# Kernel tuning notes

Measured on AMD Instinct MI355X. Metric: run time of the kernel, lower is better.

## Reference

```python
import jax, jax.numpy as jnp
import numpy as np

B, T, D = 8, 2048, 1024
GAMMA = 0.96875


def setup_inputs() -> dict:
    key = jax.random.key(0)
    ks = jax.random.split(key, 7)
    sD = 1.0 / np.sqrt(D)
    sT = 1.0 / np.sqrt(T)
    return {
        "x": jax.random.normal(ks[0], (B, T, D), dtype=jnp.float32),
        "Wq": jax.random.normal(ks[1], (D, D), dtype=jnp.float32) * sD,
        "Wk": jax.random.normal(ks[2], (D, D), dtype=jnp.float32) * sD,
        "Wv": jax.random.normal(ks[3], (D, D), dtype=jnp.float32) * sD,
        "W_ih": jax.random.normal(ks[4], (T, T), dtype=jnp.float32) * sT,
        "W_hh": jax.random.normal(ks[5], (T, T), dtype=jnp.float32) * sT,
        "b_ih": jax.random.normal(ks[6], (T,), dtype=jnp.float32) * sT,
    }


def reference(x, Wq, Wk, Wv, W_ih, W_hh, b_ih):
    # x: [B, T, D]; QKV projections (Linear with no bias: x @ W^T)
    Q = jnp.einsum("btd,ed->bte", x, Wq)
    K = jnp.einsum("btd,ed->bte", x, Wk)
    V = jnp.einsum("btd,ed->bte", x, Wv)

    # retention state injected as hidden bias of the tanh-RNN: [B, T]
    bias = jnp.sum(K * V, axis=-1)

    gamma = jnp.full((T,), GAMMA, dtype=x.dtype)
    u = gamma @ W_ih.T + b_ih  # input contribution, identical every step: [T]

    def step(h, b_t):
        h_new = jnp.tanh(u + h @ W_hh.T + b_t)
        return h_new, h_new

    h0 = jnp.zeros((T,), dtype=x.dtype)
    _, S = jax.lax.scan(step, h0, bias)  # scan over the B rows -> S: [B, T]

    # vmap(mul)(S, Q^T)^T  ==  out[b,t,d] = S[b,t] * Q[b,t,d]
    return S[:, :, None] * Q
```

## Files before the change

### kernel.cpp

```cpp
#include <hip/hip_runtime.h>
#include <stdint.h>

#define T_DIM 2048
#define D_DIM 1024
#define B_DIM 8
#define M_TOK (B_DIM * T_DIM)
#define GAMMA_C 0.96875f

typedef float f32x4 __attribute__((ext_vector_type(4)));
typedef float f32x16 __attribute__((ext_vector_type(16)));
typedef float fl4 __attribute__((ext_vector_type(4)));
typedef __bf16 bf16x8 __attribute__((ext_vector_type(8)));
typedef unsigned short us8 __attribute__((ext_vector_type(8)));
typedef unsigned short us4 __attribute__((ext_vector_type(4)));

__device__ __forceinline__ unsigned short f32_bf16_rne(float f) {
  uint32_t u = __builtin_bit_cast(uint32_t, f);
  return (unsigned short)((u + 0x7FFFu + ((u >> 16) & 1u)) >> 16);
}
__device__ __forceinline__ float bf16_f32(unsigned short h) {
  uint32_t u = ((uint32_t)h) << 16;
  return __builtin_bit_cast(float, u);
}

__device__ __forceinline__ int swz_row(int r) {
  return ((r >> 1) & 3) ^ ((r >> 3) & 3);
}

__device__ __forceinline__ void gload16(const void* g, void* l) {
  __builtin_amdgcn_global_load_lds(
      reinterpret_cast<const __attribute__((address_space(1))) uint32_t*>(
          reinterpret_cast<uintptr_t>(g)),
      reinterpret_cast<__attribute__((address_space(3))) uint32_t*>(
          reinterpret_cast<uintptr_t>(l)),
      16, 0, 0);
}

__device__ __forceinline__ bf16x8 ldfrag(const unsigned short* p) {
  us8 u = *reinterpret_cast<const us8*>(p);
  return __builtin_bit_cast(bf16x8, u);
}

#define VMW(n) asm volatile("s_waitcnt vmcnt(" #n ")" ::: "memory")
#define BAR    __builtin_amdgcn_s_barrier()

__global__ __launch_bounds__(256) void k_split(const float* __restrict__ in, int n8,
                                               unsigned short* __restrict__ hi,
                                               unsigned short* __restrict__ lo) {
  int stride = gridDim.x * blockDim.x;
  for (int i = blockIdx.x * blockDim.x + threadIdx.x; i < n8; i += stride) {
    fl4 v0 = ((const fl4*)in)[i * 2];
    fl4 v1 = ((const fl4*)in)[i * 2 + 1];
    us8 h, l;
#pragma unroll
    for (int j = 0; j < 4; ++j) {
      unsigned short hb = f32_bf16_rne(v0[j]);
      h[j] = hb;
      l[j] = f32_bf16_rne(v0[j] - bf16_f32(hb));
      unsigned short hb1 = f32_bf16_rne(v1[j]);
      h[j + 4] = hb1;
      l[j + 4] = f32_bf16_rne(v1[j] - bf16_f32(hb1));
    }
    ((us8*)hi)[i] = h;
    ((us8*)lo)[i] = l;
  }
}

__global__ __launch_bounds__(256) void k_split_hi(const float* __restrict__ in, int n8,
                                                  unsigned short* __restrict__ hi) {
  int stride = gridDim.x * blockDim.x;
  for (int i = blockIdx.x * blockDim.x + threadIdx.x; i < n8; i += stride) {
    fl4 v0 = ((const fl4*)in)[i * 2];
    fl4 v1 = ((const fl4*)in)[i * 2 + 1];
    us8 h;
#pragma unroll
    for (int j = 0; j < 4; ++j) {
      h[j] = f32_bf16_rne(v0[j]);
      h[j + 4] = f32_bf16_rne(v1[j]);
    }
    ((us8*)hi)[i] = h;
  }
}

__global__ __launch_bounds__(256) void k_split_T(const float* __restrict__ in,
                                                 unsigned short* __restrict__ th,
                                                 unsigned short* __restrict__ tl) {
  __shared__ float tile[64][69];
  int be = blockIdx.x >> 4, bd = blockIdx.x & 15;
  int e0 = be * 64, d0 = bd * 64;
  int r = threadIdx.x >> 4;
  int c = (threadIdx.x & 15) * 4;
#pragma unroll
  for (int it = 0; it < 4; ++it) {
    int rr = r + it * 16;
    fl4 v = *(const fl4*)(in + (size_t)(e0 + rr) * D_DIM + d0 + c);
#pragma unroll
    for (int j = 0; j < 4; ++j) tile[rr][c + j] = v[j];
  }
  __syncthreads();
#pragma unroll
  for (int it = 0; it < 4; ++it) {
    int dr = r + it * 16;
    us4 h, l;
#pragma unroll
    for (int j = 0; j < 4; ++j) {
      float f = tile[c + j][dr];
      h[j] = f32_bf16_rne(f);
      l[j] = f32_bf16_rne(f - bf16_f32(h[j]));
    }
    *(us4*)(th + (size_t)(d0 + dr) * D_DIM + e0 + c) = h;
    *(us4*)(tl + (size_t)(d0 + dr) * D_DIM + e0 + c) = l;
  }
}

__global__ __launch_bounds__(256) void k_u(const float* __restrict__ Wih,
                                           const float* __restrict__ bih,
                                           float* __restrict__ u) {
  int wave = threadIdx.x >> 6, lane = threadIdx.x & 63;
  int t = blockIdx.x * 4 + wave;
  const fl4* row = (const fl4*)(Wih + (size_t)t * T_DIM);
  float s = 0.f;
#pragma unroll
  for (int i = 0; i < 8; ++i) {
    fl4 v = row[lane + i * 64];
    s += v[0] + v[1] + v[2] + v[3];
  }
#pragma unroll
  for (int m = 32; m >= 1; m >>= 1) s += __shfl_xor(s, m, 64);
  if (lane == 0) u[t] = GAMMA_C * s + bih[t];
}

__global__ __launch_bounds__(256) void k_step_bf(const unsigned short* __restrict__ Whh_b,
                                                 const float* __restrict__ hprev,
                                                 const float* __restrict__ u,
                                                 const float* __restrict__ biasrow,
                                                 float* __restrict__ hout) {
  int wave = threadIdx.x >> 6, lane = threadIdx.x & 63;
  int t = blockIdx.x * 4 + wave;
  const unsigned short* row = Whh_b + (size_t)t * T_DIM;
  float s = 0.f;
#pragma unroll
  for (int i = 0; i < 4; ++i) {
    us8 w = *(const us8*)(row + i * 512 + lane * 8);
    fl4 h0 = *(const fl4*)(hprev + i * 512 + lane * 8);
    fl4 h1 = *(const fl4*)(hprev + i * 512 + lane * 8 + 4);
    s += bf16_f32(w[0]) * h0[0] + bf16_f32(w[1]) * h0[1] +
         bf16_f32(w[2]) * h0[2] + bf16_f32(w[3]) * h0[3] +
         bf16_f32(w[4]) * h1[0] + bf16_f32(w[5]) * h1[1] +
         bf16_f32(w[6]) * h1[2] + bf16_f32(w[7]) * h1[3];
  }
#pragma unroll
  for (int m = 32; m >= 1; m >>= 1) s += __shfl_xor(s, m, 64);
  if (lane == 0) hout[t] = tanhf(u[t] + s + biasrow[t]);
}

__global__ __launch_bounds__(256) void k_ht(
    const unsigned short* __restrict__ ah, const unsigned short* __restrict__ al,
    const unsigned short* __restrict__ bh, const unsigned short* __restrict__ bl,
    float* __restrict__ Hf) {
  __shared__ unsigned short sAh[2][64 * 32], sAl[2][64 * 32];
  __shared__ unsigned short sBh[2][64 * 32], sBl[2][64 * 32];
  const int tid = threadIdx.x;
  const int wave = tid >> 6, lane = tid & 63;
  const int wm = wave >> 1, wn = wave & 1;
  const int m0 = (blockIdx.x >> 4) * 64, n0 = (blockIdx.x & 15) * 64;
  const int hi32 = lane >> 5;

  const int srow = tid >> 2;
  const int csrc = (tid & 3) ^ swz_row(srow);
  const size_t ga = (size_t)(m0 + srow) * D_DIM + csrc * 8;
  const size_t gb = (size_t)(n0 + srow) * D_DIM + csrc * 8;
  const int ldst = tid * 8;

  f32x16 acc = {};
  const int l31 = lane & 31;
  const int sw = swz_row(l31);
  const int ar = wm * 32 + l31;
  const int br = wn * 32 + l31;
  int aoff[2], boff[2];
#pragma unroll
  for (int kh = 0; kh < 2; ++kh) {
    aoff[kh] = ar * 32 + (((kh * 2 + hi32) ^ sw) * 8);
    boff[kh] = br * 32 + (((kh * 2 + hi32) ^ sw) * 8);
  }

  auto stage = [&](int t, int buf) {
    const size_t ko = (size_t)t * 32;
    gload16(ah + ga + ko, &sAh[buf][ldst]);
    gload16(al + ga + ko, &sAl[buf][ldst]);
    gload16(bh + gb + ko, &sBh[buf][ldst]);
    gload16(bl + gb + ko, &sBl[buf][ldst]);
  };

  stage(0, 0);
  stage(1, 1);
  for (int kt = 0; kt < 32; ++kt) {
    const int cur = kt & 1;
    if (kt < 31) { VMW(4); } else { VMW(0); }
    BAR;
#pragma unroll
    for (int kh = 0; kh < 2; ++kh) {
      bf16x8 fah = ldfrag(&sAh[cur][aoff[kh]]);
      bf16x8 fal = ldfrag(&sAl[cur][aoff[kh]]);
      bf16x8 fbh = ldfrag(&sBh[cur][boff[kh]]);
      bf16x8 fbl = ldfrag(&sBl[cur][boff[kh]]);
      acc = __builtin_amdgcn_mfma_f32_32x32x16_bf16(fah, fbh, acc, 0, 0, 0);
      acc = __builtin_amdgcn_mfma_f32_32x32x16_bf16(fah, fbl, acc, 0, 0, 0);
      acc = __builtin_amdgcn_mfma_f32_32x32x16_bf16(fal, fbh, acc, 0, 0, 0);
    }
    BAR;
    if (kt + 2 <= 31) stage(kt + 2, cur);
  }
#pragma unroll
  for (int r = 0; r < 16; ++r) {
    int row = m0 + wm * 32 + (r & 3) + 8 * (r >> 2) + 4 * hi32;
    int col = n0 + wn * 32 + l31;
    Hf[(size_t)row * D_DIM + col] = acc[r];
  }
}

__global__ __launch_bounds__(256) void k_nprime(const float* __restrict__ Hf,
                                                unsigned short* __restrict__ mh,
                                                unsigned short* __restrict__ ml) {
  __shared__ float t2[64][65];
  const int ti = blockIdx.x >> 4;
  const int tj = blockIdx.x & 15;
  const int r0 = ti * 64, c0 = tj * 64;
  const int a = threadIdx.x >> 2;
  const int b4 = (threadIdx.x & 3) * 16;
  if (tj < ti) {
#pragma unroll
    for (int j = 0; j < 16; ++j) {
      size_t ad = (size_t)(r0 + a) * D_DIM + c0 + b4 + j;
      mh[ad] = 0;
      ml[ad] = 0;
    }
    return;
  }
#pragma unroll
  for (int j = 0; j < 16; j += 4) {
    fl4 v = *(const fl4*)(Hf + (size_t)(c0 + a) * D_DIM + r0 + b4 + j);
#pragma unroll
    for (int q = 0; q < 4; ++q) t2[a][b4 + j + q] = v[q];
  }
  __syncthreads();
#pragma unroll
  for (int j = 0; j < 16; ++j) {
    int dp = r0 + a;
    int dd = c0 + b4 + j;
    float v = 0.f;
    if (dd > dp)       v = Hf[(size_t)dp * D_DIM + dd] + t2[b4 + j][a];
    else if (dd == dp) v = Hf[(size_t)dp * D_DIM + dd];
    unsigned short hb = f32_bf16_rne(v);
    unsigned short lb = f32_bf16_rne(v - bf16_f32(hb));
    size_t ad = (size_t)dp * D_DIM + dd;
    mh[ad] = hb;
    ml[ad] = lb;
  }
}

__global__ __launch_bounds__(512, 1) void k_y_bias(
    const unsigned short* __restrict__ xh, const unsigned short* __restrict__ xl,
    const unsigned short* __restrict__ bh, const unsigned short* __restrict__ bl,
    float* __restrict__ bias) {
  __shared__ unsigned short sAh[3][128 * 32], sAl[3][128 * 32];
  __shared__ unsigned short sBh[3][256 * 32], sBl[3][256 * 32];
  const int tid = threadIdx.x;
  const int wave = tid >> 6, lane = tid & 63;
  const int wm = wave >> 2;
  const int wn = wave & 3;
  const int xcd = blockIdx.x & 7, seq = blockIdx.x >> 3;
  const int mb = xcd * 16 + (seq >> 1);
  const int half = seq & 1;
  const int m0 = mb * 128;
  const int l15 = lane & 15;
  const int kc = lane >> 4;

  const int srow = tid >> 2;
  const int csrc = (tid & 3) ^ swz_row(srow);
  const size_t gA = (size_t)(m0 + srow) * D_DIM + csrc * 8;
  const int ldstA = tid * 8;
  const int ldstB0 = tid * 8, ldstB1 = (tid + 512) * 8;

  int aoff[4], boff[4];
#pragma unroll
  for (int mi = 0; mi < 4; ++mi) {
    int r = wm * 64 + mi * 16 + l15;
    aoff[mi] = r * 32 + ((kc ^ swz_row(r)) * 8);
  }
#pragma unroll
  for (int ni = 0; ni < 4; ++ni) {
    int r = wn * 64 + ni * 16 + l15;
    boff[ni] = r * 32 + ((kc ^ swz_row(r)) * 8);
  }

  auto phase = [&](int nb, int k0, int ke) {
    const int n0 = nb * 256;
    const size_t gB0 = (size_t)(n0 + srow) * D_DIM + csrc * 8;
    const size_t gB1 = (size_t)(n0 + srow + 128) * D_DIM + csrc * 8;

    auto stage = [&](int t, int buf) {
      const size_t ko = (size_t)t * 32;
      gload16(xh + gA + ko, &sAh[buf][ldstA]);
      gload16(xl + gA + ko, &sAl[buf][ldstA]);
      gload16(bh + gB0 + ko, &sBh[buf][ldstB0]);
      gload16(bh + gB1 + ko, &sBh[buf][ldstB1]);
      gload16(bl + gB0 + ko, &sBl[buf][ldstB0]);
      gload16(bl + gB1 + ko, &sBl[buf][ldstB1]);
    };

    f32x4 acc[4][4] = {};
    BAR;
    stage(k0, 0);
    stage(k0 + 1, 1);
    int cur = 0;
    for (int kt = k0; kt < ke; ++kt) {
      if (kt < ke - 1) { VMW(6); } else { VMW(0); }
      BAR;
      int nx = cur + 2; if (nx >= 3) nx -= 3;
      if (kt + 2 < ke) stage(kt + 2, nx);
      {
        bf16x8 fah[4], fal[4];
#pragma unroll
        for (int mi = 0; mi < 4; ++mi) {
          fah[mi] = ldfrag(&sAh[cur][aoff[mi]]);
          fal[mi] = ldfrag(&sAl[cur][aoff[mi]]);
        }
#pragma unroll
        for (int nh = 0; nh < 2; ++nh) {
          bf16x8 fbh_[2], fbl_[2];
#pragma unroll
          for (int nj = 0; nj < 2; ++nj) {
            fbh_[nj] = ldfrag(&sBh[cur][boff[nh * 2 + nj]]);
            fbl_[nj] = ldfrag(&sBl[cur][boff[nh * 2 + nj]]);
          }
          __builtin_amdgcn_s_setprio(1);
#pragma unroll
          for (int mi = 0; mi < 4; ++mi)
#pragma unroll
            for (int nj = 0; nj < 2; ++nj) {
              const int ni = nh * 2 + nj;
              acc[mi][ni] = __builtin_amdgcn_mfma_f32_16x16x32_bf16(fah[mi], fbh_[nj], acc[mi][ni], 0, 0, 0);
              acc[mi][ni] = __builtin_amdgcn_mfma_f32_16x16x32_bf16(fah[mi], fbl_[nj], acc[mi][ni], 0, 0, 0);
              acc[mi][ni] = __builtin_amdgcn_mfma_f32_16x16x32_bf16(fal[mi], fbh_[nj], acc[mi][ni], 0, 0, 0);
            }
          __builtin_amdgcn_s_setprio(0);
        }
      }
      cur = cur + 1; if (cur >= 3) cur -= 3;
    }

#pragma unroll
    for (int mi = 0; mi < 4; ++mi)
#pragma unroll
      for (int j = 0; j < 4; ++j) {
        int row = m0 + wm * 64 + mi * 16 + (lane >> 4) * 4 + j;
        const size_t rb = (size_t)row * D_DIM + n0 + wn * 64 + l15;
        float p = 0.f;
#pragma unroll
        for (int ni = 0; ni < 4; ++ni) {
          float xv = bf16_f32(xh[rb + ni * 16]) + bf16_f32(xl[rb + ni * 16]);
          p += xv * acc[mi][ni][j];
        }
        p += __shfl_xor(p, 1, 64);
        p += __shfl_xor(p, 2, 64);
        p += __shfl_xor(p, 4, 64);
        p += __shfl_xor(p, 8, 64);
        if (l15 == 0) atomicAdd(&bias[row], p);
      }
  };

  if (half == 0) {
    phase(0, 0, 32);
    phase(1, 8, 16);
  } else {
    phase(1, 16, 32);
    phase(2, 16, 32);
    phase(3, 24, 32);
  }
}

__global__ __launch_bounds__(256, 4) void k_q_out(
    const unsigned short* __restrict__ xh,
    const unsigned short* __restrict__ qh_,
    const float* __restrict__ S, float* __restrict__ out) {
  __shared__ unsigned short sA[2][128 * 32];
  __shared__ unsigned short sB[2][128 * 32];
  const int tid = threadIdx.x;
  const int wave = tid >> 6, lane = tid & 63;
  const int wm = wave >> 1, wn = wave & 1;
  int sw0 = (blockIdx.x & 7) * 128 + (blockIdx.x >> 3);
  const int mb = sw0 >> 3, nb = sw0 & 7;
  const int m0 = mb * 128, n0 = nb * 128;
  const int hi32 = lane >> 5;
  const int l31 = lane & 31;

  const int srow0 = tid >> 2, srow1 = srow0 + 64;
  const int csrc0 = (tid & 3) ^ swz_row(srow0);
  const int csrc1 = (tid & 3) ^ swz_row(srow1);
  const size_t gaA0 = (size_t)(m0 + srow0) * D_DIM + csrc0 * 8;
  const size_t gaA1 = (size_t)(m0 + srow1) * D_DIM + csrc1 * 8;
  const size_t gaB0 = (size_t)(n0 + srow0) * D_DIM + csrc0 * 8;
  const size_t gaB1 = (size_t)(n0 + srow1) * D_DIM + csrc1 * 8;
  const int ldst0 = tid * 8, ldst1 = (tid + 256) * 8;

  f32x16 acc[2][2] = {};
  int aoff[2][2], boff[2][2];
#pragma unroll
  for (int mi = 0; mi < 2; ++mi) {
    int r = wm * 64 + mi * 32 + l31;
    int sw = swz_row(r);
#pragma unroll
    for (int kh = 0; kh < 2; ++kh)
      aoff[mi][kh] = r * 32 + (((kh * 2 + hi32) ^ sw) * 8);
  }
#pragma unroll
  for (int ni = 0; ni < 2; ++ni) {
    int r = wn * 64 + ni * 32 + l31;
    int sw = swz_row(r);
#pragma unroll
    for (int kh = 0; kh < 2; ++kh)
      boff[ni][kh] = r * 32 + (((kh * 2 + hi32) ^ sw) * 8);
  }

  auto stage = [&](int t, int buf) {
    const size_t ko = (size_t)t * 32;
    gload16(xh + gaA0 + ko, &sA[buf][ldst0]);
    gload16(xh + gaA1 + ko, &sA[buf][ldst1]);
    gload16(qh_ + gaB0 + ko, &sB[buf][ldst0]);
    gload16(qh_ + gaB1 + ko, &sB[buf][ldst1]);
  };

  stage(0, 0);
  stage(1, 1);
  for (int kt = 0; kt < 32; ++kt) {
    const int cur = kt & 1;
    if (kt < 31) { VMW(4); } else { VMW(0); }
    BAR;
#pragma unroll
    for (int kh = 0; kh < 2; ++kh) {
      bf16x8 fa[2], fb[2];
#pragma unroll
      for (int mi = 0; mi < 2; ++mi) fa[mi] = ldfrag(&sA[cur][aoff[mi][kh]]);
#pragma unroll
      for (int ni = 0; ni < 2; ++ni) fb[ni] = ldfrag(&sB[cur][boff[ni][kh]]);
      __builtin_amdgcn_s_setprio(1);
#pragma unroll
      for (int mi = 0; mi < 2; ++mi)
#pragma unroll
        for (int ni = 0; ni < 2; ++ni)
          acc[mi][ni] = __builtin_amdgcn_mfma_f32_32x32x16_bf16(fa[mi], fb[ni], acc[mi][ni], 0, 0, 0);
      __builtin_amdgcn_s_setprio(0);
    }
    BAR;
    if (kt + 2 <= 31) stage(kt + 2, cur);
  }

#pragma unroll
  for (int mi = 0; mi < 2; ++mi)
#pragma unroll
    for (int r = 0; r < 16; ++r) {
      int row = m0 + wm * 64 + mi * 32 + (r & 3) + 8 * (r >> 2) + 4 * hi32;
      float sc = S[row];
      float* orow = out + (size_t)row * D_DIM + n0 + wn * 64 + l31;
      orow[0] = sc * acc[mi][0][r];
      orow[32] = sc * acc[mi][1][r];
    }
}

extern "C" void kernel_launch(void* const* d_in, const int* in_sizes, int n_in,
                              void* d_out, int out_size, void* d_ws, size_t ws_size,
                              hipStream_t stream) {
  const float* x   = (const float*)d_in[0];
  const float* Wq  = (const float*)d_in[1];
  const float* Wk  = (const float*)d_in[2];
  const float* Wv  = (const float*)d_in[3];
  const float* Wih = (const float*)d_in[4];
  const float* Whh = (const float*)d_in[5];
  const float* bih = (const float*)d_in[6];
  float* out = (float*)d_out;

  char* ws = (char*)d_ws;
  size_t off = 0;
  auto alloc = [&](size_t bytes) -> char* {
    char* p = ws + off;
    off += (bytes + 255) & ~(size_t)255;
    return p;
  };
  unsigned short* xh   = (unsigned short*)alloc((size_t)M_TOK * D_DIM * 2);
  unsigned short* xl   = (unsigned short*)alloc((size_t)M_TOK * D_DIM * 2);
  unsigned short* wqh  = (unsigned short*)alloc((size_t)D_DIM * D_DIM * 2);
  unsigned short* wkth = (unsigned short*)alloc((size_t)D_DIM * D_DIM * 2);
  unsigned short* wktl = (unsigned short*)alloc((size_t)D_DIM * D_DIM * 2);
  unsigned short* wvth = (unsigned short*)alloc((size_t)D_DIM * D_DIM * 2);
  unsigned short* wvtl = (unsigned short*)alloc((size_t)D_DIM * D_DIM * 2);
  unsigned short* mph  = (unsigned short*)alloc((size_t)D_DIM * D_DIM * 2);
  unsigned short* mpl  = (unsigned short*)alloc((size_t)D_DIM * D_DIM * 2);
  float* Hf   = (float*)alloc((size_t)D_DIM * D_DIM * 4);
  float* bias = (float*)alloc((size_t)M_TOK * 4);
  float* Sbuf = (float*)alloc((size_t)M_TOK * 4);
  float* ubuf = (float*)alloc((size_t)T_DIM * 4);
  float* zbuf = (float*)alloc((size_t)T_DIM * 4);
  unsigned short* whhb = wkth;
  (void)ws_size; (void)in_sizes; (void)n_in; (void)out_size;

  k_split<<<2048, 256, 0, stream>>>(x, M_TOK * D_DIM / 8, xh, xl);
  k_split_hi<<<512, 256, 0, stream>>>(Wq, D_DIM * D_DIM / 8, wqh);
  k_split_T<<<256, 256, 0, stream>>>(Wk, wkth, wktl);
  k_split_T<<<256, 256, 0, stream>>>(Wv, wvth, wvtl);

  hipMemsetAsync(bias, 0, (size_t)M_TOK * 4, stream);
  hipMemsetAsync(zbuf, 0, (size_t)T_DIM * 4, stream);

  k_u<<<T_DIM / 4, 256, 0, stream>>>(Wih, bih, ubuf);

  k_ht<<<256, 256, 0, stream>>>(wvth, wvtl, wkth, wktl, Hf);

  k_nprime<<<256, 256, 0, stream>>>(Hf, mph, mpl);

  k_split_hi<<<1024, 256, 0, stream>>>(Whh, T_DIM * T_DIM / 8, whhb);

  k_y_bias<<<256, 512, 0, stream>>>(xh, xl, mph, mpl, bias);

  for (int b = 0; b < B_DIM; ++b) {
    const float* hp = (b == 0) ? zbuf : (Sbuf + (size_t)(b - 1) * T_DIM);
    k_step_bf<<<T_DIM / 4, 256, 0, stream>>>(whhb, hp, ubuf, bias + (size_t)b * T_DIM,
                                             Sbuf + (size_t)b * T_DIM);
  }

  k_q_out<<<1024, 256, 0, stream>>>(xh, wqh, Sbuf, out);
}
```

Before: 238.6 us.

## Enlarge k_y_bias tile to 256x256 with 1024 threads and double buffering

Restructures the bias GEMM kernel to use 1024-thread blocks, each covering a 256-row M tile instead of 128. The LDS pipeline goes from triple to double buffering, with an extra barrier before the next prefetch. The upper-triangular work is rebalanced across four quarters per M block instead of two halves. The aim is better reuse of the B tile and more even work per block, at the cost of less prefetch depth, an added barrier per k-step, and tighter per-thread register budget.

```diff
diff --git a/kernel.cpp b/kernel.cpp
--- a/kernel.cpp
+++ b/kernel.cpp
@@ -43,6 +43,7 @@
 
 #define VMW(n) asm volatile("s_waitcnt vmcnt(" #n ")" ::: "memory")
 #define BAR    __builtin_amdgcn_s_barrier()
+#define MEMFENCE asm volatile("" ::: "memory")
 
 __global__ __launch_bounds__(256) void k_split(const float* __restrict__ in, int n8,
                                                unsigned short* __restrict__ hi,
@@ -259,28 +260,27 @@
   }
 }
 
-__global__ __launch_bounds__(512, 1) void k_y_bias(
+__global__ __launch_bounds__(1024, 1) void k_y_bias(
     const unsigned short* __restrict__ xh, const unsigned short* __restrict__ xl,
     const unsigned short* __restrict__ bh, const unsigned short* __restrict__ bl,
     float* __restrict__ bias) {
-  __shared__ unsigned short sAh[3][128 * 32], sAl[3][128 * 32];
-  __shared__ unsigned short sBh[3][256 * 32], sBl[3][256 * 32];
+  __shared__ unsigned short sAh[2][256 * 32], sAl[2][256 * 32];
+  __shared__ unsigned short sBh[2][256 * 32], sBl[2][256 * 32];
   const int tid = threadIdx.x;
   const int wave = tid >> 6, lane = tid & 63;
   const int wm = wave >> 2;
   const int wn = wave & 3;
   const int xcd = blockIdx.x & 7, seq = blockIdx.x >> 3;
-  const int mb = xcd * 16 + (seq >> 1);
-  const int half = seq & 1;
-  const int m0 = mb * 128;
+  const int mb = xcd * 8 + (seq >> 2);
+  const int quarter = seq & 3;
+  const int m0 = mb * 256;
   const int l15 = lane & 15;
   const int kc = lane >> 4;
 
   const int srow = tid >> 2;
   const int csrc = (tid & 3) ^ swz_row(srow);
   const size_t gA = (size_t)(m0 + srow) * D_DIM + csrc * 8;
-  const int ldstA = tid * 8;
-  const int ldstB0 = tid * 8, ldstB1 = (tid + 512) * 8;
+  const int ldst = tid * 8;
 
   int aoff[4], boff[4];
 #pragma unroll
@@ -296,35 +296,31 @@
 
   auto phase = [&](int nb, int k0, int ke) {
     const int n0 = nb * 256;
-    const size_t gB0 = (size_t)(n0 + srow) * D_DIM + csrc * 8;
-    const size_t gB1 = (size_t)(n0 + srow + 128) * D_DIM + csrc * 8;
+    const size_t gB = (size_t)(n0 + srow) * D_DIM + csrc * 8;
 
     auto stage = [&](int t, int buf) {
       const size_t ko = (size_t)t * 32;
-      gload16(xh + gA + ko, &sAh[buf][ldstA]);
-      gload16(xl + gA + ko, &sAl[buf][ldstA]);
-      gload16(bh + gB0 + ko, &sBh[buf][ldstB0]);
-      gload16(bh + gB1 + ko, &sBh[buf][ldstB1]);
-      gload16(bl + gB0 + ko, &sBl[buf][ldstB0]);
-      gload16(bl + gB1 + ko, &sBl[buf][ldstB1]);
+      gload16(xh + gA + ko, &sAh[buf][ldst]);
+      gload16(xl + gA + ko, &sAl[buf][ldst]);
+      gload16(bh + gB + ko, &sBh[buf][ldst]);
+      gload16(bl + gB + ko, &sBl[buf][ldst]);
     };
 
     f32x4 acc[4][4] = {};
     BAR;
     stage(k0, 0);
     stage(k0 + 1, 1);
-    int cur = 0;
     for (int kt = k0; kt < ke; ++kt) {
-      if (kt < ke - 1) { VMW(6); } else { VMW(0); }
+      const int cur = (kt - k0) & 1;
+      if (kt < ke - 1) { VMW(4); } else { VMW(0); }
       BAR;
-      int nx = cur + 2; if (nx >= 3) nx -= 3;
-      if (kt + 2 < ke) stage(kt + 2, nx);
-      {
-        bf16x8 fah[4], fal[4];
-#pragma unroll
-        for (int mi = 0; mi < 4; ++mi) {
-          fah[mi] = ldfrag(&sAh[cur][aoff[mi]]);
-          fal[mi] = ldfrag(&sAl[cur][aoff[mi]]);
+#pragma unroll
+      for (int mh = 0; mh < 2; ++mh) {
+        bf16x8 fah[2], fal[2];
+#pragma unroll
+        for (int mj = 0; mj < 2; ++mj) {
+          fah[mj] = ldfrag(&sAh[cur][aoff[mh * 2 + mj]]);
+          fal[mj] = ldfrag(&sAl[cur][aoff[mh * 2 + mj]]);
         }
 #pragma unroll
         for (int nh = 0; nh < 2; ++nh) {
@@ -336,18 +332,20 @@
           }
           __builtin_amdgcn_s_setprio(1);
 #pragma unroll
-          for (int mi = 0; mi < 4; ++mi)
+          for (int mj = 0; mj < 2; ++mj)
 #pragma unroll
             for (int nj = 0; nj < 2; ++nj) {
-              const int ni = nh * 2 + nj;
-              acc[mi][ni] = __builtin_amdgcn_mfma_f32_16x16x32_bf16(fah[mi], fbh_[nj], acc[mi][ni], 0, 0, 0);
-              acc[mi][ni] = __builtin_amdgcn_mfma_f32_16x16x32_bf16(fah[mi], fbl_[nj], acc[mi][ni], 0, 0, 0);
-              acc[mi][ni] = __builtin_amdgcn_mfma_f32_16x16x32_bf16(fal[mi], fbh_[nj], acc[mi][ni], 0, 0, 0);
+              const int mi = mh * 2 + mj, ni = nh * 2 + nj;
+              acc[mi][ni] = __builtin_amdgcn_mfma_f32_16x16x32_bf16(fah[mj], fbh_[nj], acc[mi][ni], 0, 0, 0);
+              acc[mi][ni] = __builtin_amdgcn_mfma_f32_16x16x32_bf16(fah[mj], fbl_[nj], acc[mi][ni], 0, 0, 0);
+              acc[mi][ni] = __builtin_amdgcn_mfma_f32_16x16x32_bf16(fal[mj], fbh_[nj], acc[mi][ni], 0, 0, 0);
             }
           __builtin_amdgcn_s_setprio(0);
+          MEMFENCE;
         }
       }
-      cur = cur + 1; if (cur >= 3) cur -= 3;
+      BAR;
+      if (kt + 2 < ke) stage(kt + 2, cur);
     }
 
 #pragma unroll
@@ -370,12 +368,16 @@
       }
   };
 
-  if (half == 0) {
-    phase(0, 0, 32);
+  if (quarter == 0) {
+    phase(0, 0, 20);
+  } else if (quarter == 1) {
+    phase(0, 20, 32);
     phase(1, 8, 16);
+  } else if (quarter == 2) {
+    phase(1, 16, 32);
+    phase(2, 16, 20);
   } else {
-    phase(1, 16, 32);
-    phase(2, 16, 32);
+    phase(2, 20, 32);
     phase(3, 24, 32);
   }
 }
@@ -520,7 +522,7 @@
 
   k_split_hi<<<1024, 256, 0, stream>>>(Whh, T_DIM * T_DIM / 8, whhb);
 
-  k_y_bias<<<256, 512, 0, stream>>>(xh, xl, mph, mpl, bias);
+  k_y_bias<<<256, 1024, 0, stream>>>(xh, xl, mph, mpl, bias);
 
   for (int b = 0; b < B_DIM; ++b) {
     const float* hp = (b == 0) ? zbuf : (Sbuf + (size_t)(b - 1) * T_DIM);
```

After: 269.5 us. 12.9% more time.
